# Kernel optimization log

Measured on AMD Instinct MI355X. Metric: run time of the kernel, lower is better.

## Reference

```python
import jax, jax.numpy as jnp
import numpy as np

N_NODES = 50000
N_EDGES = 600000
IN_DIM = 128
OUT_DIM = 128
EPS = 1e-5


def setup_inputs() -> dict:
    key = jax.random.key(0)
    k1, k2, k3 = jax.random.split(key, 3)
    h = jax.random.normal(k1, (N_NODES, IN_DIM), dtype=jnp.float32)
    edge_index = jax.random.randint(k2, (2, N_EDGES), 0, N_NODES, dtype=jnp.int64)
    ln_gamma = jnp.ones((IN_DIM,), dtype=jnp.float32)
    ln_beta = jnp.zeros((IN_DIM,), dtype=jnp.float32)
    W = jax.random.normal(k3, (OUT_DIM, 2 * IN_DIM), dtype=jnp.float32) * (1.0 / np.sqrt(2 * IN_DIM))
    b = jnp.zeros((OUT_DIM,), dtype=jnp.float32)
    return {"h": h, "edge_index": edge_index, "ln_gamma": ln_gamma,
            "ln_beta": ln_beta, "W": W, "b": b}


def _layernorm(x, gamma, beta):
    mu = jnp.mean(x, axis=-1, keepdims=True)
    var = jnp.mean(jnp.square(x - mu), axis=-1, keepdims=True)
    return (x - mu) * jax.lax.rsqrt(var + EPS) * gamma + beta


def reference(h, edge_index, ln_gamma, ln_beta, W, b):
    src, dst = edge_index[0], edge_index[1]
    n = h.shape[0]
    # LayerNorm
    hn = _layernorm(h, ln_gamma, ln_beta)  # [N, D]
    # Degrees (DGL norm='both' clamps to min 1)
    ones = jnp.ones((src.shape[0],), dtype=h.dtype)
    deg_out = jnp.clip(jax.ops.segment_sum(ones, src, num_segments=n), 1.0)
    deg_in = jnp.clip(jax.ops.segment_sum(ones, dst, num_segments=n), 1.0)
    inv_sqrt_out = jax.lax.rsqrt(deg_out)  # [N]
    inv_sqrt_in = jax.lax.rsqrt(deg_in)    # [N]
    # SpMM: message = D_in^{-1/2} A D_out^{-1/2} hn
    msg_src = hn * inv_sqrt_out[:, None]                 # scale at source
    gathered = msg_src[src]                              # [E, D] irregular gather
    agg = jax.ops.segment_sum(gathered, dst, num_segments=n)  # [N, D]
    message = agg * inv_sqrt_in[:, None]
    # Concat + Linear (dropout is identity in eval)
    cat = jnp.concatenate([hn, message], axis=1)  # [N, 2D]
    return cat @ W.T + b
```

## Files before the change

### kernel.cpp

```cpp
#include <hip/hip_runtime.h>
#include <stdint.h>

#define N_NODES 50000
#define N_EDGES 600000
#define D       128
#define EPS     1e-5f
#define HG      32
#define NWORDS  25000

typedef __attribute__((ext_vector_type(8))) short bf16x8;
typedef __attribute__((ext_vector_type(4))) float f32x4;

__device__ __forceinline__ unsigned short f2bf(float x) {
    unsigned int u = __float_as_uint(x);
    return (unsigned short)((u + 0x7fffu + ((u >> 16) & 1u)) >> 16);
}

__device__ __forceinline__ int load_idx(const void* e, long long i, int is64) {
    return is64 ? (int)((const long long*)e)[i] : ((const int*)e)[i];
}

__device__ __forceinline__ int block_detect64(const unsigned int* eraw, int* sflag) {
    if (threadIdx.x < 64) {
        unsigned long long nz = __ballot(eraw[2 * threadIdx.x + 1] != 0u);
        if (threadIdx.x == 0) *sflag = (nz == 0ull) ? 1 : 0;
    }
    __syncthreads();
    return *sflag;
}

__global__ __launch_bounds__(1024) void hist_kernel(const unsigned int* __restrict__ eraw,
                                                    unsigned int* __restrict__ partials,
                                                    const float2* __restrict__ W2,
                                                    unsigned int* __restrict__ Wb) {
    __shared__ unsigned int lhist[NWORDS];
    __shared__ int sflag;
    int t = threadIdx.x;
    int which = blockIdx.x >= HG;
    int b     = blockIdx.x & (HG - 1);
    for (int i = t; i < NWORDS; i += 1024) lhist[i] = 0u;
    int is64 = block_detect64(eraw, &sflag);
    const int per = N_EDGES / HG;
    int lo = b * per, hi = lo + per;
    long long base = which ? (long long)N_EDGES : 0ll;
    for (int i = lo + t; i < hi; i += 1024) {
        int v = load_idx(eraw, base + i, is64);
        atomicAdd(&lhist[v >> 1], (v & 1) ? (1u << 16) : 1u);
    }
    __syncthreads();
    unsigned int* dst = partials + (size_t)blockIdx.x * NWORDS;
    for (int i = t; i < NWORDS; i += 1024) dst[i] = lhist[i];
    if (blockIdx.x == 0) {
        for (int i = t; i < 128 * 128; i += 1024) {
            float2 w = W2[i];
            Wb[i] = (unsigned int)f2bf(w.x) | ((unsigned int)f2bf(w.y) << 16);
        }
    }
}

__global__ __launch_bounds__(256) void deg_reduce(const unsigned int* __restrict__ partials,
                                                  unsigned int* __restrict__ deg_in,
                                                  float* __restrict__ inv_out,
                                                  float* __restrict__ inv_in) {
    int w = blockIdx.x * 256 + threadIdx.x;
    if (w >= NWORDS) return;
    unsigned int o0 = 0, o1 = 0, d0 = 0, d1 = 0;
    for (int b = 0; b < HG; ++b) {
        unsigned int p = partials[(size_t)b * NWORDS + w];
        o0 += p & 0xffffu; o1 += p >> 16;
    }
    for (int b = 0; b < HG; ++b) {
        unsigned int p = partials[(size_t)(HG + b) * NWORDS + w];
        d0 += p & 0xffffu; d1 += p >> 16;
    }
    deg_in[2 * w]     = d0;
    deg_in[2 * w + 1] = d1;
    inv_out[2 * w]     = rsqrtf((float)(o0 > 1u ? o0 : 1u));
    inv_out[2 * w + 1] = rsqrtf((float)(o1 > 1u ? o1 : 1u));
    inv_in[2 * w]      = rsqrtf((float)(d0 > 1u ? d0 : 1u));
    inv_in[2 * w + 1]  = rsqrtf((float)(d1 > 1u ? d1 : 1u));
}

__global__ __launch_bounds__(1024) void scan1(const unsigned int* __restrict__ deg,
                                              unsigned int* __restrict__ row_start,
                                              unsigned int* __restrict__ partials) {
    __shared__ unsigned int wsum[16];
    int t = threadIdx.x, lane = t & 63, w = t >> 6;
    int i = blockIdx.x * 1024 + t;
    unsigned int v = (i < N_NODES) ? deg[i] : 0u;
    unsigned int x = v;
    #pragma unroll
    for (int off = 1; off < 64; off <<= 1) {
        unsigned int y = __shfl_up(x, off, 64);
        if (lane >= off) x += y;
    }
    if (lane == 63) wsum[w] = x;
    __syncthreads();
    if (w == 0) {
        unsigned int s = (lane < 16) ? wsum[lane] : 0u;
        #pragma unroll
        for (int off = 1; off < 16; off <<= 1) {
            unsigned int y = __shfl_up(s, off, 64);
            if (lane >= off) s += y;
        }
        if (lane < 16) wsum[lane] = s;
    }
    __syncthreads();
    unsigned int excl = (w ? wsum[w - 1] : 0u) + x - v;
    if (i < N_NODES) row_start[i] = excl;
    if (t == 1023) partials[blockIdx.x] = wsum[15];
}

__global__ __launch_bounds__(1024) void scan2(const unsigned int* __restrict__ partials,
                                              unsigned int* __restrict__ row_start) {
    __shared__ unsigned int soff;
    int t = threadIdx.x, b = blockIdx.x;
    if (t < 64) {
        unsigned int p = (t < b) ? partials[t] : 0u;
        #pragma unroll
        for (int off = 32; off; off >>= 1) p += __shfl_xor(p, off, 64);
        if (t == 0) soff = p;
    }
    __syncthreads();
    int i = b * 1024 + t;
    if (i < N_NODES) row_start[i] += soff;
    if (b == 0 && t == 0) row_start[N_NODES] = N_EDGES;
}

__global__ __launch_bounds__(256) void prefix_kernel(const unsigned int* __restrict__ partials,
                                                     const unsigned int* __restrict__ row_start,
                                                     unsigned int* __restrict__ pre) {
    int w = blockIdx.x * 256 + threadIdx.x;
    if (w >= NWORDS) return;
    unsigned int run0 = row_start[2 * w], run1 = row_start[2 * w + 1];
    for (int b = 0; b < HG; ++b) {
        pre[(size_t)b * N_NODES + 2 * w]     = run0;
        pre[(size_t)b * N_NODES + 2 * w + 1] = run1;
        unsigned int p = partials[(size_t)(HG + b) * NWORDS + w];
        run0 += p & 0xffffu; run1 += p >> 16;
    }
}

__global__ __launch_bounds__(1024) void fill_kernel(const unsigned int* __restrict__ eraw,
                                                    const unsigned int* __restrict__ pre,
                                                    unsigned int* __restrict__ csr_src) {
    __shared__ unsigned int lcur[NWORDS];
    __shared__ int sflag;
    int t = threadIdx.x, b = blockIdx.x;
    for (int i = t; i < NWORDS; i += 1024) lcur[i] = 0u;
    int is64 = block_detect64(eraw, &sflag);
    const int per = N_EDGES / HG;
    int lo = b * per, hi = lo + per;
    const unsigned int* preb = pre + (size_t)b * N_NODES;
    for (int i = lo + t; i < hi; i += 1024) {
        int s = load_idx(eraw, i, is64);
        int d = load_idx(eraw, (long long)N_EDGES + i, is64);
        unsigned int old = atomicAdd(&lcur[d >> 1], (d & 1) ? (1u << 16) : 1u);
        unsigned int pl = (d & 1) ? (old >> 16) : (old & 0xffffu);
        csr_src[preb[d] + pl] = (unsigned int)s;
    }
}

__global__ __launch_bounds__(256) void ln_kernel(const float2* __restrict__ h2,
                                                 const float2* __restrict__ g2,
                                                 const float2* __restrict__ b2,
                                                 unsigned int* __restrict__ hnb) {
    int wid  = threadIdx.x >> 6;
    int lane = threadIdx.x & 63;
    int row  = blockIdx.x * 4 + wid;
    if (row >= N_NODES) return;
    float2 v = h2[(size_t)row * 64 + lane];
    float s  = v.x + v.y;
    float ss = v.x * v.x + v.y * v.y;
    #pragma unroll
    for (int off = 32; off; off >>= 1) {
        s  += __shfl_xor(s,  off, 64);
        ss += __shfl_xor(ss, off, 64);
    }
    float mu  = s * (1.0f / D);
    float var = ss * (1.0f / D) - mu * mu;
    float rs  = rsqrtf(var + EPS);
    float2 g = g2[lane], b = b2[lane];
    float y0 = (v.x - mu) * rs * g.x + b.x;
    float y1 = (v.y - mu) * rs * g.y + b.y;
    hnb[(size_t)row * 64 + lane] = (unsigned int)f2bf(y0) | ((unsigned int)f2bf(y1) << 16);
}

__global__ __launch_bounds__(256) void agg_kernel(const unsigned int* __restrict__ hnb,
                                                  const float* __restrict__ inv_out,
                                                  const float* __restrict__ inv_in,
                                                  const unsigned int* __restrict__ row_start,
                                                  const unsigned int* __restrict__ csr_src,
                                                  unsigned int* __restrict__ aggb) {
    int wid  = threadIdx.x >> 6;
    int lane = threadIdx.x & 63;
    int row  = blockIdx.x * 4 + wid;
    if (row >= N_NODES) return;
    int g = lane >> 4, gl = lane & 15;
    unsigned int e0 = row_start[row], e1 = row_start[row + 1];
    float acc[8];
    #pragma unroll
    for (int j = 0; j < 8; ++j) acc[j] = 0.0f;

    unsigned int e = e0;
    while (e < e1) {
        unsigned int cnt = e1 - e;
        if (cnt > 64u) cnt = 64u;
        int sl = (lane < (int)cnt) ? (int)csr_src[e + lane] : 0;
        int nit = ((int)cnt + 3) >> 2;
        for (int it = 0; it < nit; ++it) {
            int idx = it * 4 + g;
            int s = __shfl(sl, idx, 64);
            if (idx < (int)cnt) {
                float sc = inv_out[s];
                uint4 v = *(const uint4*)(hnb + (size_t)s * 64 + gl * 4);
                acc[0] = fmaf(__uint_as_float(v.x << 16),          sc, acc[0]);
                acc[1] = fmaf(__uint_as_float(v.x & 0xffff0000u),  sc, acc[1]);
                acc[2] = fmaf(__uint_as_float(v.y << 16),          sc, acc[2]);
                acc[3] = fmaf(__uint_as_float(v.y & 0xffff0000u),  sc, acc[3]);
                acc[4] = fmaf(__uint_as_float(v.z << 16),          sc, acc[4]);
                acc[5] = fmaf(__uint_as_float(v.z & 0xffff0000u),  sc, acc[5]);
                acc[6] = fmaf(__uint_as_float(v.w << 16),          sc, acc[6]);
                acc[7] = fmaf(__uint_as_float(v.w & 0xffff0000u),  sc, acc[7]);
            }
        }
        e += cnt;
    }
    #pragma unroll
    for (int j = 0; j < 8; ++j) {
        acc[j] += __shfl_xor(acc[j], 16, 64);
        acc[j] += __shfl_xor(acc[j], 32, 64);
    }
    if (g == 0) {
        float ii = inv_in[row];
        uint4 o;
        o.x = (unsigned int)f2bf(acc[0] * ii) | ((unsigned int)f2bf(acc[1] * ii) << 16);
        o.y = (unsigned int)f2bf(acc[2] * ii) | ((unsigned int)f2bf(acc[3] * ii) << 16);
        o.z = (unsigned int)f2bf(acc[4] * ii) | ((unsigned int)f2bf(acc[5] * ii) << 16);
        o.w = (unsigned int)f2bf(acc[6] * ii) | ((unsigned int)f2bf(acc[7] * ii) << 16);
        *(uint4*)(aggb + (size_t)row * 64 + gl * 4) = o;
    }
}

__global__ __launch_bounds__(256) void gemm_kernel(const unsigned short* __restrict__ hnb,
                                                   const unsigned short* __restrict__ aggb,
                                                   const unsigned short* __restrict__ Wb,
                                                   const float* __restrict__ bias,
                                                   float* __restrict__ out) {
    __shared__ unsigned short wlds[128 * 264];
    int t = threadIdx.x;
    {
        int j = t >> 1, half = t & 1;
        const uint4* src = (const uint4*)(Wb + (size_t)j * 256 + half * 128);
        uint4* dst = (uint4*)(wlds + j * 264 + half * 128);
        #pragma unroll
        for (int i = 0; i < 16; ++i) dst[i] = src[i];
    }
    __syncthreads();

    int w = t >> 6, lane = t & 63;
    int rbase = blockIdx.x * 64 + w * 16;
    if (rbase >= N_NODES) return;
    int lrow = lane & 15, lhi = lane >> 4;

    bf16x8 a[8];
    const unsigned short* hrow = hnb + (size_t)(rbase + lrow) * 128 + lhi * 8;
    const unsigned short* arow = aggb + (size_t)(rbase + lrow) * 128 + lhi * 8;
    #pragma unroll
    for (int kc = 0; kc < 4; ++kc) a[kc]     = *(const bf16x8*)(hrow + kc * 32);
    #pragma unroll
    for (int kc = 0; kc < 4; ++kc) a[4 + kc] = *(const bf16x8*)(arow + kc * 32);

    f32x4 acc[8];
    #pragma unroll
    for (int ct = 0; ct < 8; ++ct) acc[ct] = (f32x4){0.f, 0.f, 0.f, 0.f};

    #pragma unroll
    for (int ct = 0; ct < 8; ++ct) {
        const unsigned short* bb = wlds + (ct * 16 + lrow) * 264 + lhi * 8;
        #pragma unroll
        for (int kc = 0; kc < 8; ++kc) {
            bf16x8 bfrag = *(const bf16x8*)(bb + kc * 32);
            acc[ct] = __builtin_amdgcn_mfma_f32_16x16x32_bf16(a[kc], bfrag, acc[ct], 0, 0, 0);
        }
    }

    #pragma unroll
    for (int ct = 0; ct < 8; ++ct) {
        int col = ct * 16 + lrow;
        float bv = bias[col];
        #pragma unroll
        for (int i = 0; i < 4; ++i) {
            int row = rbase + lhi * 4 + i;
            out[(size_t)row * 128 + col] = acc[ct][i] + bv;
        }
    }
}

extern "C" void kernel_launch(void* const* d_in, const int* in_sizes, int n_in,
                              void* d_out, int out_size, void* d_ws, size_t ws_size,
                              hipStream_t stream) {
    const float* h     = (const float*)d_in[0];
    const unsigned int* eraw = (const unsigned int*)d_in[1];
    const float* gamma = (const float*)d_in[2];
    const float* beta  = (const float*)d_in[3];
    const float* W     = (const float*)d_in[4];
    const float* bias  = (const float*)d_in[5];
    float* out = (float*)d_out;

    char* ws = (char*)d_ws;
    size_t off = 0;
    auto alloc = [&](size_t bytes) { size_t o = off; off += (bytes + 255) & ~(size_t)255; return o; };
    unsigned int* hpart     = (unsigned int*)(ws + alloc((size_t)2 * HG * NWORDS * 4));
    unsigned int* pre       = (unsigned int*)(ws + alloc((size_t)HG * N_NODES * 4));
    unsigned int* deg_in    = (unsigned int*)(ws + alloc((size_t)N_NODES * 4));
    float*        inv_out   = (float*)(ws + alloc((size_t)N_NODES * 4));
    float*        inv_in    = (float*)(ws + alloc((size_t)N_NODES * 4));
    unsigned int* row_start = (unsigned int*)(ws + alloc((size_t)(N_NODES + 1) * 4));
    unsigned int* spart     = (unsigned int*)(ws + alloc(64 * 4));
    unsigned int* Wb        = (unsigned int*)(ws + alloc((size_t)128 * 256 * 2));
    unsigned int* csr_src   = (unsigned int*)(ws + alloc((size_t)N_EDGES * 4));
    unsigned int* hnb       = (unsigned int*)(ws + alloc((size_t)N_NODES * D * 2));
    unsigned int* aggb      = (unsigned int*)(ws + alloc((size_t)N_NODES * D * 2));

    hist_kernel<<<2 * HG, 1024, 0, stream>>>(eraw, hpart, (const float2*)W, Wb);
    ln_kernel<<<(N_NODES + 3) / 4, 256, 0, stream>>>((const float2*)h, (const float2*)gamma,
                                                     (const float2*)beta, hnb);
    deg_reduce<<<(NWORDS + 255) / 256, 256, 0, stream>>>(hpart, deg_in, inv_out, inv_in);
    scan1<<<(N_NODES + 1023) / 1024, 1024, 0, stream>>>(deg_in, row_start, spart);
    scan2<<<(N_NODES + 1023) / 1024, 1024, 0, stream>>>(spart, row_start);
    prefix_kernel<<<(NWORDS + 255) / 256, 256, 0, stream>>>(hpart, row_start, pre);
    fill_kernel<<<HG, 1024, 0, stream>>>(eraw, pre, csr_src);
    agg_kernel<<<(N_NODES + 3) / 4, 256, 0, stream>>>(hnb, inv_out, inv_in, row_start,
                                                      csr_src, aggb);
    gemm_kernel<<<(N_NODES + 63) / 64, 256, 0, stream>>>((const unsigned short*)hnb,
                                                         (const unsigned short*)aggb,
                                                         (const unsigned short*)Wb,
                                                         bias, out);
}
```

Measured before the change: 125.1 us.

## Widen histogram/fill grid, fuse per-block prefix into degree reduce, use 16-bit CSR

The histogram and CSR-fill stages go from 32 to 128 edge chunks, so more workgroups run in these otherwise underused kernels. The per-block prefix offsets are now built inside the degree-reduction kernel as packed 16-bit relative offsets, which removes the separate prefix kernel. Fill adds row_start to those offsets. CSR source indices are stored as 16-bit values to halve index traffic in fill and aggregation. In exchange, the reduction reads four times as many partial histograms, and correctness relies on node ids and per-node partial counts fitting in 16 bits.

```diff
diff --git a/kernel.cpp b/kernel.cpp
--- a/kernel.cpp
+++ b/kernel.cpp
@@ -5,7 +5,8 @@
 #define N_EDGES 600000
 #define D       128
 #define EPS     1e-5f
-#define HG      32
+#define HG      128
+#define PER     ((N_EDGES + HG - 1) / HG)
 #define NWORDS  25000
 
 typedef __attribute__((ext_vector_type(8))) short bf16x8;
@@ -37,11 +38,11 @@
     __shared__ int sflag;
     int t = threadIdx.x;
     int which = blockIdx.x >= HG;
-    int b     = blockIdx.x & (HG - 1);
+    int b     = blockIdx.x - (which ? HG : 0);
     for (int i = t; i < NWORDS; i += 1024) lhist[i] = 0u;
     int is64 = block_detect64(eraw, &sflag);
-    const int per = N_EDGES / HG;
-    int lo = b * per, hi = lo + per;
+    int lo = b * PER;
+    int hi = lo + PER; if (hi > N_EDGES) hi = N_EDGES;
     long long base = which ? (long long)N_EDGES : 0ll;
     for (int i = lo + t; i < hi; i += 1024) {
         int v = load_idx(eraw, base + i, is64);
@@ -58,27 +59,30 @@
     }
 }
 
-__global__ __launch_bounds__(256) void deg_reduce(const unsigned int* __restrict__ partials,
-                                                  unsigned int* __restrict__ deg_in,
-                                                  float* __restrict__ inv_out,
-                                                  float* __restrict__ inv_in) {
+__global__ __launch_bounds__(256) void reduce_prefix(const unsigned int* __restrict__ partials,
+                                                     unsigned int* __restrict__ deg_in,
+                                                     float* __restrict__ inv_out,
+                                                     float* __restrict__ inv_in,
+                                                     unsigned int* __restrict__ pre16) {
     int w = blockIdx.x * 256 + threadIdx.x;
     if (w >= NWORDS) return;
-    unsigned int o0 = 0, o1 = 0, d0 = 0, d1 = 0;
+    unsigned int o0 = 0, o1 = 0;
     for (int b = 0; b < HG; ++b) {
         unsigned int p = partials[(size_t)b * NWORDS + w];
         o0 += p & 0xffffu; o1 += p >> 16;
     }
+    unsigned int run0 = 0, run1 = 0;
     for (int b = 0; b < HG; ++b) {
+        pre16[(size_t)b * NWORDS + w] = run0 | (run1 << 16);
         unsigned int p = partials[(size_t)(HG + b) * NWORDS + w];
-        d0 += p & 0xffffu; d1 += p >> 16;
-    }
-    deg_in[2 * w]     = d0;
-    deg_in[2 * w + 1] = d1;
+        run0 += p & 0xffffu; run1 += p >> 16;
+    }
+    deg_in[2 * w]     = run0;
+    deg_in[2 * w + 1] = run1;
     inv_out[2 * w]     = rsqrtf((float)(o0 > 1u ? o0 : 1u));
     inv_out[2 * w + 1] = rsqrtf((float)(o1 > 1u ? o1 : 1u));
-    inv_in[2 * w]      = rsqrtf((float)(d0 > 1u ? d0 : 1u));
-    inv_in[2 * w + 1]  = rsqrtf((float)(d1 > 1u ? d1 : 1u));
+    inv_in[2 * w]      = rsqrtf((float)(run0 > 1u ? run0 : 1u));
+    inv_in[2 * w + 1]  = rsqrtf((float)(run1 > 1u ? run1 : 1u));
 }
 
 __global__ __launch_bounds__(1024) void scan1(const unsigned int* __restrict__ deg,
@@ -127,37 +131,26 @@
     if (b == 0 && t == 0) row_start[N_NODES] = N_EDGES;
 }
 
-__global__ __launch_bounds__(256) void prefix_kernel(const unsigned int* __restrict__ partials,
-                                                     const unsigned int* __restrict__ row_start,
-                                                     unsigned int* __restrict__ pre) {
-    int w = blockIdx.x * 256 + threadIdx.x;
-    if (w >= NWORDS) return;
-    unsigned int run0 = row_start[2 * w], run1 = row_start[2 * w + 1];
-    for (int b = 0; b < HG; ++b) {
-        pre[(size_t)b * N_NODES + 2 * w]     = run0;
-        pre[(size_t)b * N_NODES + 2 * w + 1] = run1;
-        unsigned int p = partials[(size_t)(HG + b) * NWORDS + w];
-        run0 += p & 0xffffu; run1 += p >> 16;
-    }
-}
-
 __global__ __launch_bounds__(1024) void fill_kernel(const unsigned int* __restrict__ eraw,
-                                                    const unsigned int* __restrict__ pre,
-                                                    unsigned int* __restrict__ csr_src) {
+                                                    const unsigned int* __restrict__ pre16,
+                                                    const unsigned int* __restrict__ row_start,
+                                                    unsigned short* __restrict__ csr16) {
     __shared__ unsigned int lcur[NWORDS];
     __shared__ int sflag;
     int t = threadIdx.x, b = blockIdx.x;
     for (int i = t; i < NWORDS; i += 1024) lcur[i] = 0u;
     int is64 = block_detect64(eraw, &sflag);
-    const int per = N_EDGES / HG;
-    int lo = b * per, hi = lo + per;
-    const unsigned int* preb = pre + (size_t)b * N_NODES;
+    int lo = b * PER;
+    int hi = lo + PER; if (hi > N_EDGES) hi = N_EDGES;
+    const unsigned int* preb = pre16 + (size_t)b * NWORDS;
     for (int i = lo + t; i < hi; i += 1024) {
         int s = load_idx(eraw, i, is64);
         int d = load_idx(eraw, (long long)N_EDGES + i, is64);
         unsigned int old = atomicAdd(&lcur[d >> 1], (d & 1) ? (1u << 16) : 1u);
-        unsigned int pl = (d & 1) ? (old >> 16) : (old & 0xffffu);
-        csr_src[preb[d] + pl] = (unsigned int)s;
+        unsigned int pl  = (d & 1) ? (old >> 16) : (old & 0xffffu);
+        unsigned int pw  = preb[d >> 1];
+        unsigned int pv  = (d & 1) ? (pw >> 16) : (pw & 0xffffu);
+        csr16[row_start[d] + pv + pl] = (unsigned short)s;
     }
 }
 
@@ -190,7 +183,7 @@
                                                   const float* __restrict__ inv_out,
                                                   const float* __restrict__ inv_in,
                                                   const unsigned int* __restrict__ row_start,
-                                                  const unsigned int* __restrict__ csr_src,
+                                                  const unsigned short* __restrict__ csr16,
                                                   unsigned int* __restrict__ aggb) {
     int wid  = threadIdx.x >> 6;
     int lane = threadIdx.x & 63;
@@ -206,7 +199,7 @@
     while (e < e1) {
         unsigned int cnt = e1 - e;
         if (cnt > 64u) cnt = 64u;
-        int sl = (lane < (int)cnt) ? (int)csr_src[e + lane] : 0;
+        int sl = (lane < (int)cnt) ? (int)csr16[e + lane] : 0;
         int nit = ((int)cnt + 3) >> 2;
         for (int it = 0; it < nit; ++it) {
             int idx = it * 4 + g;
@@ -311,28 +304,28 @@
     char* ws = (char*)d_ws;
     size_t off = 0;
     auto alloc = [&](size_t bytes) { size_t o = off; off += (bytes + 255) & ~(size_t)255; return o; };
-    unsigned int* hpart     = (unsigned int*)(ws + alloc((size_t)2 * HG * NWORDS * 4));
-    unsigned int* pre       = (unsigned int*)(ws + alloc((size_t)HG * N_NODES * 4));
-    unsigned int* deg_in    = (unsigned int*)(ws + alloc((size_t)N_NODES * 4));
-    float*        inv_out   = (float*)(ws + alloc((size_t)N_NODES * 4));
-    float*        inv_in    = (float*)(ws + alloc((size_t)N_NODES * 4));
-    unsigned int* row_start = (unsigned int*)(ws + alloc((size_t)(N_NODES + 1) * 4));
-    unsigned int* spart     = (unsigned int*)(ws + alloc(64 * 4));
-    unsigned int* Wb        = (unsigned int*)(ws + alloc((size_t)128 * 256 * 2));
-    unsigned int* csr_src   = (unsigned int*)(ws + alloc((size_t)N_EDGES * 4));
-    unsigned int* hnb       = (unsigned int*)(ws + alloc((size_t)N_NODES * D * 2));
-    unsigned int* aggb      = (unsigned int*)(ws + alloc((size_t)N_NODES * D * 2));
+    unsigned int*  hpart     = (unsigned int*)(ws + alloc((size_t)2 * HG * NWORDS * 4));
+    unsigned int*  pre16     = (unsigned int*)(ws + alloc((size_t)HG * NWORDS * 4));
+    unsigned int*  deg_in    = (unsigned int*)(ws + alloc((size_t)N_NODES * 4));
+    float*         inv_out   = (float*)(ws + alloc((size_t)N_NODES * 4));
+    float*         inv_in    = (float*)(ws + alloc((size_t)N_NODES * 4));
+    unsigned int*  row_start = (unsigned int*)(ws + alloc((size_t)(N_NODES + 1) * 4));
+    unsigned int*  spart     = (unsigned int*)(ws + alloc(64 * 4));
+    unsigned int*  Wb        = (unsigned int*)(ws + alloc((size_t)128 * 256 * 2));
+    unsigned short* csr16    = (unsigned short*)(ws + alloc((size_t)N_EDGES * 2));
+    unsigned int*  hnb       = (unsigned int*)(ws + alloc((size_t)N_NODES * D * 2));
+    unsigned int*  aggb      = (unsigned int*)(ws + alloc((size_t)N_NODES * D * 2));
 
     hist_kernel<<<2 * HG, 1024, 0, stream>>>(eraw, hpart, (const float2*)W, Wb);
     ln_kernel<<<(N_NODES + 3) / 4, 256, 0, stream>>>((const float2*)h, (const float2*)gamma,
                                                      (const float2*)beta, hnb);
-    deg_reduce<<<(NWORDS + 255) / 256, 256, 0, stream>>>(hpart, deg_in, inv_out, inv_in);
+    reduce_prefix<<<(NWORDS + 255) / 256, 256, 0, stream>>>(hpart, deg_in, inv_out,
+                                                            inv_in, pre16);
     scan1<<<(N_NODES + 1023) / 1024, 1024, 0, stream>>>(deg_in, row_start, spart);
     scan2<<<(N_NODES + 1023) / 1024, 1024, 0, stream>>>(spart, row_start);
-    prefix_kernel<<<(NWORDS + 255) / 256, 256, 0, stream>>>(hpart, row_start, pre);
-    fill_kernel<<<HG, 1024, 0, stream>>>(eraw, pre, csr_src);
+    fill_kernel<<<HG, 1024, 0, stream>>>(eraw, pre16, row_start, csr16);
     agg_kernel<<<(N_NODES + 3) / 4, 256, 0, stream>>>(hnb, inv_out, inv_in, row_start,
-                                                      csr_src, aggb);
+                                                      csr16, aggb);
     gemm_kernel<<<(N_NODES + 63) / 64, 256, 0, stream>>>((const unsigned short*)hnb,
                                                          (const unsigned short*)aggb,
                                                          (const unsigned short*)Wb,
```

New measurement: 108.2 us (median of 2 runs). 13.5% less time.
